# Optimization experiments

Hardware: AMD Instinct MI355X
Metric: run time of the kernel (lower is better)

Reference implementation:

```python
import jax, jax.numpy as jnp
import numpy as np

B, C, H, Wd = 16, 256, 64, 64
D_MODEL = 256


def setup_inputs() -> dict:
    key = jax.random.key(0)
    kx, kw = jax.random.split(key)
    x = jax.random.normal(kx, (B, C, H, Wd), dtype=jnp.float32)
    # 1x1 conv weight [out_c=1+2*d_model, in_c], scaled like kaiming-ish init
    W = jax.random.normal(kw, (1 + 2 * D_MODEL, C), dtype=jnp.float32) / np.sqrt(C)
    return {"x": x, "W": W}


def reference(x, W):
    b, c, h, w = x.shape
    d = (W.shape[0] - 1) // 2
    n = h * w
    xf = x.reshape(b, c, n)                      # [b, c, N]
    qkv = jnp.einsum('oc,bcn->bon', W, xf)       # 1x1 conv == channel GEMM
    q = qkv[:, :1]                               # [b, 1, N]
    k = qkv[:, 1:1 + d]                          # [b, d, N]
    v = qkv[:, 1 + d:]                           # [b, d, N]
    scores = jax.nn.softmax(q, axis=-1)          # softmax over tokens
    ctx = jnp.sum(k * scores, axis=-1, keepdims=True)  # [b, d, 1]
    out = jax.nn.relu(v) * ctx                   # gated ReLU(v)
    return out.reshape(b, d, h, w)
```

## Files before the change

### kernel.cpp

```cpp
#include <hip/hip_runtime.h>
#include <cstdint>
#include <cstddef>

#define NB 16
#define NC 256
#define NN 4096
#define ND 256

typedef unsigned short u16;
typedef unsigned int u32;

typedef __attribute__((ext_vector_type(8))) short short8;
typedef __attribute__((ext_vector_type(4))) float f32x4;

__device__ __forceinline__ u16 f2bf(float f) {
  union { float f; u32 u; } v; v.f = f;
  u32 r = v.u + 0x7FFFu + ((v.u >> 16) & 1u);
  return (u16)(r >> 16);
}
__device__ __forceinline__ float bf2f(u16 h) {
  union { u32 u; float f; } v; v.u = ((u32)h) << 16; return v.f;
}

__global__ __launch_bounds__(256) void k_init(const float* __restrict__ W,
                                              float* __restrict__ q,
                                              float* __restrict__ xs,
                                              u16* __restrict__ wvb) {
  const int blk = blockIdx.x, t = threadIdx.x;
  if (blk < 272) {
    const int i = blk * 256 + t;
    if (i < NB * NN) q[i] = 0.f;
    else xs[i - NB * NN] = 0.f;
  } else {
    const int i = ((blk - 272) * 256 + t) * 4;
    const float4 v = *(const float4*)(W + (size_t)(1 + ND) * NC + i);
    ushort4 o;
    o.x = f2bf(v.x); o.y = f2bf(v.y); o.z = f2bf(v.z); o.w = f2bf(v.w);
    *(ushort4*)(wvb + i) = o;
  }
}

__global__ __launch_bounds__(256) void k_cast_transpose_q(const float* __restrict__ x,
                                                          const float* __restrict__ W,
                                                          u16* __restrict__ xbT,
                                                          float* __restrict__ q) {
  __shared__ __align__(16) u16 tile[64 * 68];
  __shared__ float qred[16 * 64];
  const int t = threadIdx.x;
  const int b = blockIdx.z, c0 = blockIdx.y * 64, n0 = blockIdx.x * 64;
  const float* xb = x + (size_t)(b * NC + c0) * NN + n0;
  const int nl = (t & 15) * 4;
  float qacc[4] = {0.f, 0.f, 0.f, 0.f};
#pragma unroll
  for (int i = 0; i < 4; ++i) {
    int cl = (t >> 4) + i * 16;
    float4 v = *(const float4*)(xb + (size_t)cl * NN + nl);
    const float wq = W[c0 + cl];
    qacc[0] += wq * v.x; qacc[1] += wq * v.y;
    qacc[2] += wq * v.z; qacc[3] += wq * v.w;
    tile[(nl + 0) * 68 + cl] = f2bf(v.x);
    tile[(nl + 1) * 68 + cl] = f2bf(v.y);
    tile[(nl + 2) * 68 + cl] = f2bf(v.z);
    tile[(nl + 3) * 68 + cl] = f2bf(v.w);
  }
#pragma unroll
  for (int j = 0; j < 4; ++j) qred[(t >> 4) * 64 + nl + j] = qacc[j];
  __syncthreads();
  u16* ob = xbT + (size_t)(b * NN + n0) * NC + c0;
#pragma unroll
  for (int i = 0; i < 4; ++i) {
    int e = t + i * 256;
    int rn = e >> 4;
    int rc = (e & 15) * 4;
    ushort4 pv = *(const ushort4*)&tile[rn * 68 + rc];
    *(ushort4*)(ob + (size_t)rn * NC + rc) = pv;
  }
  if (t < 64) {
    float s = 0.f;
#pragma unroll
    for (int k = 0; k < 16; ++k) s += qred[k * 64 + t];
    atomicAdd(&q[b * NN + n0 + t], s);
  }
}

__global__ __launch_bounds__(1024) void k_softmax(const float* __restrict__ q,
                                                  float* __restrict__ s) {
  __shared__ float redm[16];
  __shared__ float redz[16];
  const int b = blockIdx.x, t = threadIdx.x;
  const int wave = t >> 6, lane = t & 63;
  float4 v = *(const float4*)(q + (size_t)b * NN + t * 4);
  float m = fmaxf(fmaxf(v.x, v.y), fmaxf(v.z, v.w));
#pragma unroll
  for (int off = 32; off > 0; off >>= 1) m = fmaxf(m, __shfl_down(m, off));
  if (lane == 0) redm[wave] = m;
  __syncthreads();
  float M = redm[0];
#pragma unroll
  for (int k = 1; k < 16; ++k) M = fmaxf(M, redm[k]);
  float4 e;
  e.x = __expf(v.x - M); e.y = __expf(v.y - M);
  e.z = __expf(v.z - M); e.w = __expf(v.w - M);
  float sum = e.x + e.y + e.z + e.w;
#pragma unroll
  for (int off = 32; off > 0; off >>= 1) sum += __shfl_down(sum, off);
  if (lane == 0) redz[wave] = sum;
  __syncthreads();
  float Z = 0.f;
#pragma unroll
  for (int k = 0; k < 16; ++k) Z += redz[k];
  const float inv = 1.f / Z;
  e.x *= inv; e.y *= inv; e.z *= inv; e.w *= inv;
  *(float4*)(s + (size_t)b * NN + t * 4) = e;
}

__global__ __launch_bounds__(256) void k_xs(const u16* __restrict__ xbT,
                                            const float* __restrict__ s,
                                            float* __restrict__ xs) {
  __shared__ float red[4 * 256];
  const int t = threadIdx.x;
  const int b = blockIdx.y, n0 = blockIdx.x * 128;
  const int w = t >> 6, c4 = (t & 63) * 4;
  const u16* xp = xbT + ((size_t)(b * NN + n0 + w * 32)) * NC + c4;
  const float* sp = s + b * NN + n0 + w * 32;
  float a0 = 0.f, a1 = 0.f, a2 = 0.f, a3 = 0.f;
#pragma unroll 8
  for (int j = 0; j < 32; ++j) {
    ushort4 v = *(const ushort4*)(xp + (size_t)j * NC);
    float sv = sp[j];
    a0 += bf2f(v.x) * sv; a1 += bf2f(v.y) * sv;
    a2 += bf2f(v.z) * sv; a3 += bf2f(v.w) * sv;
  }
  red[w * 256 + c4 + 0] = a0; red[w * 256 + c4 + 1] = a1;
  red[w * 256 + c4 + 2] = a2; red[w * 256 + c4 + 3] = a3;
  __syncthreads();
  float sum = red[t] + red[256 + t] + red[512 + t] + red[768 + t];
  atomicAdd(&xs[b * NC + t], sum);
}

__global__ __launch_bounds__(256) void k_ctx(const float* __restrict__ W,
                                             const float* __restrict__ xs,
                                             float* __restrict__ ctx) {
  __shared__ float sx[NC];
  const int b = blockIdx.x, d = threadIdx.x;
  sx[d] = xs[b * NC + d];
  __syncthreads();
  const float* wk = W + (size_t)(1 + d) * NC;
  float acc = 0.f;
#pragma unroll 4
  for (int c = 0; c < NC; ++c) acc += wk[c] * sx[c];
  ctx[b * NC + d] = acc;
}

__global__ __launch_bounds__(256) void k_gemm(const u16* __restrict__ xbT,
                                              const u16* __restrict__ wvb,
                                              const float* __restrict__ ctx,
                                              float* __restrict__ out) {
  const int t = threadIdx.x;
  const int b = blockIdx.z;
  const int d0 = blockIdx.y * 64;
  const int n0 = blockIdx.x * 256;
  const int lane = t & 63, w = t >> 6;
  const int wn = w * 64;
  const int quad = lane >> 4, l15 = lane & 15;

  const u16* pA = wvb + (size_t)(d0 + l15) * NC + quad * 8;
  const u16* pB = xbT + (size_t)(b * NN + n0 + wn + l15) * NC + quad * 8;

  f32x4 acc[4][4];
#pragma unroll
  for (int mi = 0; mi < 4; ++mi)
#pragma unroll
    for (int ni = 0; ni < 4; ++ni)
      acc[mi][ni] = (f32x4){0.f, 0.f, 0.f, 0.f};

  short8 af[2][4], bfr[2][4];
#pragma unroll
  for (int mi = 0; mi < 4; ++mi) af[0][mi] = *(const short8*)(pA + (size_t)mi * 16 * NC);
#pragma unroll
  for (int ni = 0; ni < 4; ++ni) bfr[0][ni] = *(const short8*)(pB + (size_t)ni * 16 * NC);

#pragma unroll
  for (int kt = 1; kt < 8; ++kt) {
    const int cur = (kt - 1) & 1, nxt = kt & 1;
    const int kk = kt * 32;
#pragma unroll
    for (int mi = 0; mi < 4; ++mi)
      af[nxt][mi] = *(const short8*)(pA + (size_t)mi * 16 * NC + kk);
#pragma unroll
    for (int ni = 0; ni < 4; ++ni)
      bfr[nxt][ni] = *(const short8*)(pB + (size_t)ni * 16 * NC + kk);
#pragma unroll
    for (int mi = 0; mi < 4; ++mi)
#pragma unroll
      for (int ni = 0; ni < 4; ++ni)
        acc[mi][ni] = __builtin_amdgcn_mfma_f32_16x16x32_bf16(af[cur][mi], bfr[cur][ni],
                                                              acc[mi][ni], 0, 0, 0);
  }
#pragma unroll
  for (int mi = 0; mi < 4; ++mi)
#pragma unroll
    for (int ni = 0; ni < 4; ++ni)
      acc[mi][ni] = __builtin_amdgcn_mfma_f32_16x16x32_bf16(af[1][mi], bfr[1][ni],
                                                            acc[mi][ni], 0, 0, 0);

#pragma unroll
  for (int mi = 0; mi < 4; ++mi) {
#pragma unroll
    for (int r = 0; r < 4; ++r) {
      const int d = d0 + mi * 16 + quad * 4 + r;
      const float cx = ctx[b * NC + d];
      float* op = out + (size_t)(b * NC + d) * NN + n0 + wn + l15;
#pragma unroll
      for (int ni = 0; ni < 4; ++ni) {
        float v = acc[mi][ni][r];
        op[ni * 16] = fmaxf(v, 0.f) * cx;
      }
    }
  }
}

extern "C" void kernel_launch(void* const* d_in, const int* in_sizes, int n_in,
                              void* d_out, int out_size, void* d_ws, size_t ws_size,
                              hipStream_t stream) {
  const float* x = (const float*)d_in[0];
  const float* W = (const float*)d_in[1];
  float* out = (float*)d_out;

  char* ws = (char*)d_ws;
  u16* xbT   = (u16*)ws;
  float* q   = (float*)(ws + 33554432);
  float* s   = (float*)(ws + 33554432 + 262144);
  float* xs  = (float*)(ws + 33554432 + 524288);
  float* ctx = (float*)(ws + 33554432 + 540672);
  u16* wvb   = (u16*)(ws + 33554432 + 557056);

  k_init<<<336, 256, 0, stream>>>(W, q, xs, wvb);
  k_cast_transpose_q<<<dim3(64, 4, 16), 256, 0, stream>>>(x, W, xbT, q);
  k_softmax<<<16, 1024, 0, stream>>>(q, s);
  k_xs<<<dim3(32, 16), 256, 0, stream>>>(xbT, s, xs);
  k_ctx<<<16, 256, 0, stream>>>(W, xs, ctx);
  k_gemm<<<dim3(16, 4, 16), 256, 0, stream>>>(xbT, wvb, ctx, out);
}
```

Measured before the change: 169.1 us.

## Stage GEMM tiles through LDS with async loads and fuse ctx computation

Result: faster. 161.9 us (-4.3%).

```diff
diff --git a/kernel.cpp b/kernel.cpp
--- a/kernel.cpp
+++ b/kernel.cpp
@@ -138,34 +138,54 @@
   atomicAdd(&xs[b * NC + t], sum);
 }
 
-__global__ __launch_bounds__(256) void k_ctx(const float* __restrict__ W,
-                                             const float* __restrict__ xs,
-                                             float* __restrict__ ctx) {
-  __shared__ float sx[NC];
-  const int b = blockIdx.x, d = threadIdx.x;
-  sx[d] = xs[b * NC + d];
-  __syncthreads();
-  const float* wk = W + (size_t)(1 + d) * NC;
-  float acc = 0.f;
-#pragma unroll 4
-  for (int c = 0; c < NC; ++c) acc += wk[c] * sx[c];
-  ctx[b * NC + d] = acc;
-}
+#define BK 32
 
 __global__ __launch_bounds__(256) void k_gemm(const u16* __restrict__ xbT,
                                               const u16* __restrict__ wvb,
-                                              const float* __restrict__ ctx,
+                                              const float* __restrict__ W,
+                                              const float* __restrict__ xs,
                                               float* __restrict__ out) {
+  __shared__ __align__(16) u16 As[2][128 * BK];
+  __shared__ __align__(16) u16 Bs[2][128 * BK];
+  __shared__ float ctxred[256];
   const int t = threadIdx.x;
   const int b = blockIdx.z;
-  const int d0 = blockIdx.y * 64;
-  const int n0 = blockIdx.x * 256;
+  const int d0 = blockIdx.y * 128;
+  const int n0 = blockIdx.x * 128;
   const int lane = t & 63, w = t >> 6;
-  const int wn = w * 64;
+  const int wd = (w & 1) * 64, wn = (w >> 1) * 64;
   const int quad = lane >> 4, l15 = lane & 15;
 
-  const u16* pA = wvb + (size_t)(d0 + l15) * NC + quad * 8;
-  const u16* pB = xbT + (size_t)(b * NN + n0 + wn + l15) * NC + quad * 8;
+  const int rstg = t >> 2;
+  const int l8 = ((t & 3) ^ (rstg & 3)) * 8;
+  const u16* gA = wvb + (size_t)(d0 + rstg) * NC + l8;
+  const u16* gB = xbT + (size_t)(b * NN + n0 + rstg) * NC + l8;
+  const int ldst = 8 * t;
+
+#define STAGE(buf, kk)                                                          \
+  do {                                                                          \
+    _Pragma("unroll")                                                           \
+    for (int i = 0; i < 2; ++i) {                                               \
+      __builtin_amdgcn_global_load_lds(                                         \
+          (const __attribute__((address_space(1))) u32*)(gA + (kk) + (size_t)(64 * i) * NC), \
+          (__attribute__((address_space(3))) u32*)(As[buf] + 2048 * i + ldst), 16, 0, 0);    \
+      __builtin_amdgcn_global_load_lds(                                         \
+          (const __attribute__((address_space(1))) u32*)(gB + (kk) + (size_t)(64 * i) * NC), \
+          (__attribute__((address_space(3))) u32*)(Bs[buf] + 2048 * i + ldst), 16, 0, 0);    \
+    }                                                                           \
+  } while (0)
+
+  STAGE(0, 0);
+
+  {
+    const int dl = t >> 1, half = t & 1;
+    const float* wk = W + (size_t)(1 + d0 + dl) * NC + half * 128;
+    const float* xp = xs + b * NC + half * 128;
+    float a = 0.f;
+#pragma unroll 8
+    for (int j = 0; j < 128; ++j) a += wk[j] * xp[j];
+    ctxred[t] = a;
+  }
 
   f32x4 acc[4][4];
 #pragma unroll
@@ -174,43 +194,35 @@
     for (int ni = 0; ni < 4; ++ni)
       acc[mi][ni] = (f32x4){0.f, 0.f, 0.f, 0.f};
 
-  short8 af[2][4], bfr[2][4];
-#pragma unroll
-  for (int mi = 0; mi < 4; ++mi) af[0][mi] = *(const short8*)(pA + (size_t)mi * 16 * NC);
-#pragma unroll
-  for (int ni = 0; ni < 4; ++ni) bfr[0][ni] = *(const short8*)(pB + (size_t)ni * 16 * NC);
-
-#pragma unroll
-  for (int kt = 1; kt < 8; ++kt) {
-    const int cur = (kt - 1) & 1, nxt = kt & 1;
-    const int kk = kt * 32;
+  const int pq = (quad ^ (l15 & 3)) * 8;
+
+#pragma unroll
+  for (int kt = 0; kt < 8; ++kt) {
+    const int buf = kt & 1;
+    __syncthreads();
+    if (kt < 7) STAGE(buf ^ 1, (kt + 1) * BK);
+    short8 af[4], bfr[4];
 #pragma unroll
     for (int mi = 0; mi < 4; ++mi)
-      af[nxt][mi] = *(const short8*)(pA + (size_t)mi * 16 * NC + kk);
+      af[mi] = *(const short8*)&As[buf][(wd + mi * 16 + l15) * BK + pq];
 #pragma unroll
     for (int ni = 0; ni < 4; ++ni)
-      bfr[nxt][ni] = *(const short8*)(pB + (size_t)ni * 16 * NC + kk);
+      bfr[ni] = *(const short8*)&Bs[buf][(wn + ni * 16 + l15) * BK + pq];
 #pragma unroll
     for (int mi = 0; mi < 4; ++mi)
 #pragma unroll
       for (int ni = 0; ni < 4; ++ni)
-        acc[mi][ni] = __builtin_amdgcn_mfma_f32_16x16x32_bf16(af[cur][mi], bfr[cur][ni],
+        acc[mi][ni] = __builtin_amdgcn_mfma_f32_16x16x32_bf16(af[mi], bfr[ni],
                                                               acc[mi][ni], 0, 0, 0);
   }
-#pragma unroll
-  for (int mi = 0; mi < 4; ++mi)
-#pragma unroll
-    for (int ni = 0; ni < 4; ++ni)
-      acc[mi][ni] = __builtin_amdgcn_mfma_f32_16x16x32_bf16(af[1][mi], bfr[1][ni],
-                                                            acc[mi][ni], 0, 0, 0);
 
 #pragma unroll
   for (int mi = 0; mi < 4; ++mi) {
 #pragma unroll
     for (int r = 0; r < 4; ++r) {
-      const int d = d0 + mi * 16 + quad * 4 + r;
-      const float cx = ctx[b * NC + d];
-      float* op = out + (size_t)(b * NC + d) * NN + n0 + wn + l15;
+      const int dl = wd + mi * 16 + quad * 4 + r;
+      const float cx = ctxred[2 * dl] + ctxred[2 * dl + 1];
+      float* op = out + (size_t)(b * NC + d0 + dl) * NN + n0 + wn + l15;
 #pragma unroll
       for (int ni = 0; ni < 4; ++ni) {
         float v = acc[mi][ni][r];
@@ -218,6 +230,7 @@
       }
     }
   }
+#undef STAGE
 }
 
 extern "C" void kernel_launch(void* const* d_in, const int* in_sizes, int n_in,
@@ -232,13 +245,11 @@
   float* q   = (float*)(ws + 33554432);
   float* s   = (float*)(ws + 33554432 + 262144);
   float* xs  = (float*)(ws + 33554432 + 524288);
-  float* ctx = (float*)(ws + 33554432 + 540672);
   u16* wvb   = (u16*)(ws + 33554432 + 557056);
 
   k_init<<<336, 256, 0, stream>>>(W, q, xs, wvb);
   k_cast_transpose_q<<<dim3(64, 4, 16), 256, 0, stream>>>(x, W, xbT, q);
   k_softmax<<<16, 1024, 0, stream>>>(q, s);
   k_xs<<<dim3(32, 16), 256, 0, stream>>>(xbT, s, xs);
-  k_ctx<<<16, 256, 0, stream>>>(W, xs, ctx);
-  k_gemm<<<dim3(16, 4, 16), 256, 0, stream>>>(xbT, wvb, ctx, out);
-}
+  k_gemm<<<dim3(32, 2, 16), 256, 0, stream>>>(xbT, wvb, W, xs, out);
+}
```

## Restructure value GEMM with register-resident weights and LDS-staged swizzled activation tiles

Applied to the files above, without the earlier changes.

Measured after the change: 166.4 us. Within noise of the previous version (-1.6%).

```diff
diff --git a/kernel.cpp b/kernel.cpp
--- a/kernel.cpp
+++ b/kernel.cpp
@@ -152,71 +152,83 @@
   ctx[b * NC + d] = acc;
 }
 
-__global__ __launch_bounds__(256) void k_gemm(const u16* __restrict__ xbT,
-                                              const u16* __restrict__ wvb,
-                                              const float* __restrict__ ctx,
-                                              float* __restrict__ out) {
+#define GW 512
+
+__global__ __launch_bounds__(256, 2) void k_gemm(const u16* __restrict__ xbT,
+                                                 const u16* __restrict__ wvb,
+                                                 const float* __restrict__ ctx,
+                                                 float* __restrict__ out) {
+  __shared__ __align__(16) u16 Bs[64 * 256];
   const int t = threadIdx.x;
-  const int b = blockIdx.z;
-  const int d0 = blockIdx.y * 64;
-  const int n0 = blockIdx.x * 256;
   const int lane = t & 63, w = t >> 6;
-  const int wn = w * 64;
   const int quad = lane >> 4, l15 = lane & 15;
 
-  const u16* pA = wvb + (size_t)(d0 + l15) * NC + quad * 8;
-  const u16* pB = xbT + (size_t)(b * NN + n0 + wn + l15) * NC + quad * 8;
-
-  f32x4 acc[4][4];
-#pragma unroll
-  for (int mi = 0; mi < 4; ++mi)
-#pragma unroll
-    for (int ni = 0; ni < 4; ++ni)
-      acc[mi][ni] = (f32x4){0.f, 0.f, 0.f, 0.f};
-
-  short8 af[2][4], bfr[2][4];
-#pragma unroll
-  for (int mi = 0; mi < 4; ++mi) af[0][mi] = *(const short8*)(pA + (size_t)mi * 16 * NC);
-#pragma unroll
-  for (int ni = 0; ni < 4; ++ni) bfr[0][ni] = *(const short8*)(pB + (size_t)ni * 16 * NC);
-
-#pragma unroll
-  for (int kt = 1; kt < 8; ++kt) {
-    const int cur = (kt - 1) & 1, nxt = kt & 1;
-    const int kk = kt * 32;
+  short8 af[4][8];
+  {
+    const u16* pA = wvb + (size_t)(64 * w + l15) * NC + quad * 8;
 #pragma unroll
     for (int mi = 0; mi < 4; ++mi)
-      af[nxt][mi] = *(const short8*)(pA + (size_t)mi * 16 * NC + kk);
-#pragma unroll
-    for (int ni = 0; ni < 4; ++ni)
-      bfr[nxt][ni] = *(const short8*)(pB + (size_t)ni * 16 * NC + kk);
+#pragma unroll
+      for (int kt = 0; kt < 8; ++kt)
+        af[mi][kt] = *(const short8*)(pA + (size_t)mi * 16 * NC + kt * 32);
+  }
+
+  const int pstg = t & 31;
+  const int rbase = t >> 5;
+
+#pragma unroll 1
+  for (int a = 0; a < 2; ++a) {
+    const int tau = a * GW + blockIdx.x;
+    const int b = tau >> 6;
+    const int n0 = (tau & 63) * 64;
+
+#pragma unroll
+    for (int j = 0; j < 8; ++j) {
+      const int row = j * 8 + rbase;
+      const int c = pstg ^ (row & 7);
+      __builtin_amdgcn_global_load_lds(
+          (const __attribute__((address_space(1))) u32*)(xbT + (size_t)(b * NN + n0 + row) * NC + c * 8),
+          (__attribute__((address_space(3))) u32*)(Bs + j * 2048 + t * 8), 16, 0, 0);
+    }
+    __syncthreads();
+
+    f32x4 acc[4][4];
 #pragma unroll
     for (int mi = 0; mi < 4; ++mi)
 #pragma unroll
       for (int ni = 0; ni < 4; ++ni)
-        acc[mi][ni] = __builtin_amdgcn_mfma_f32_16x16x32_bf16(af[cur][mi], bfr[cur][ni],
-                                                              acc[mi][ni], 0, 0, 0);
-  }
-#pragma unroll
-  for (int mi = 0; mi < 4; ++mi)
-#pragma unroll
-    for (int ni = 0; ni < 4; ++ni)
-      acc[mi][ni] = __builtin_amdgcn_mfma_f32_16x16x32_bf16(af[1][mi], bfr[1][ni],
-                                                            acc[mi][ni], 0, 0, 0);
-
-#pragma unroll
-  for (int mi = 0; mi < 4; ++mi) {
-#pragma unroll
-    for (int r = 0; r < 4; ++r) {
-      const int d = d0 + mi * 16 + quad * 4 + r;
-      const float cx = ctx[b * NC + d];
-      float* op = out + (size_t)(b * NC + d) * NN + n0 + wn + l15;
+        acc[mi][ni] = (f32x4){0.f, 0.f, 0.f, 0.f};
+
+#pragma unroll
+    for (int kt = 0; kt < 8; ++kt) {
+      short8 bfr[4];
 #pragma unroll
       for (int ni = 0; ni < 4; ++ni) {
-        float v = acc[mi][ni][r];
-        op[ni * 16] = fmaxf(v, 0.f) * cx;
+        const int row = ni * 16 + l15;
+        const int pc = (kt * 4 + quad) ^ (l15 & 7);
+        bfr[ni] = *(const short8*)&Bs[row * 256 + pc * 8];
+      }
+#pragma unroll
+      for (int mi = 0; mi < 4; ++mi)
+#pragma unroll
+        for (int ni = 0; ni < 4; ++ni)
+          acc[mi][ni] = __builtin_amdgcn_mfma_f32_16x16x32_bf16(af[mi][kt], bfr[ni],
+                                                                acc[mi][ni], 0, 0, 0);
+    }
+
+#pragma unroll
+    for (int mi = 0; mi < 4; ++mi) {
+#pragma unroll
+      for (int r = 0; r < 4; ++r) {
+        const int d = 64 * w + mi * 16 + quad * 4 + r;
+        const float cx = ctx[b * NC + d];
+        float* op = out + (size_t)(b * NC + d) * NN + n0 + l15;
+#pragma unroll
+        for (int ni = 0; ni < 4; ++ni)
+          op[ni * 16] = fmaxf(acc[mi][ni][r], 0.f) * cx;
       }
     }
+    __syncthreads();
   }
 }
 
@@ -240,5 +252,5 @@
   k_softmax<<<16, 1024, 0, stream>>>(q, s);
   k_xs<<<dim3(32, 16), 256, 0, stream>>>(xbT, s, xs);
   k_ctx<<<16, 256, 0, stream>>>(W, xs, ctx);
-  k_gemm<<<dim3(16, 4, 16), 256, 0, stream>>>(xbT, wvb, ctx, out);
-}
+  k_gemm<<<GW, 256, 0, stream>>>(xbT, wvb, ctx, out);
+}
```
